# Optimization experiments

Measured on AMD Instinct MI355X. Metric: run time of the kernel, lower is better.

The kernel has to match this reference:

```python
import jax, jax.numpy as jnp
import numpy as np

B, T = 2, 2048
N_EMBED = 2048
N_HEAD = 16
N_KV_HEAD = 4
HEAD_DIM = N_EMBED // N_HEAD  # 128
KV_DIM = HEAD_DIM * N_KV_HEAD  # 512
REPEAT = N_HEAD // N_KV_HEAD  # 4
THETA = 10000.0


def _apply_rope(x):
    # x: (B, T, H, D), interleaved-pair rotation as in RotaryEmbedding
    D = x.shape[-1]
    inv_freq = 1.0 / (THETA ** (jnp.arange(0, D, 2, dtype=jnp.float32) / D))  # (D/2,)
    t = jnp.arange(x.shape[1], dtype=jnp.float32)
    freqs = t[:, None] * inv_freq[None, :]            # (T, D/2)
    cos = jnp.cos(freqs)[None, :, None, :]            # (1, T, 1, D/2)
    sin = jnp.sin(freqs)[None, :, None, :]
    x1 = x[..., ::2]
    x2 = x[..., 1::2]
    even = x1 * cos - x2 * sin
    odd = x1 * sin + x2 * cos
    out = jnp.stack([even, odd], axis=-1)             # (B, T, H, D/2, 2)
    return out.reshape(x.shape)


def setup_inputs() -> dict:
    key = jax.random.key(0)
    ks = jax.random.split(key, 9)
    s_in = 1.0 / np.sqrt(N_EMBED)
    return {
        "x": jax.random.normal(ks[0], (B, T, N_EMBED), dtype=jnp.float32),
        "Wq": jax.random.normal(ks[1], (N_EMBED, N_EMBED), dtype=jnp.float32) * s_in,
        "bq": jax.random.normal(ks[2], (N_EMBED,), dtype=jnp.float32) * 0.01,
        "Wk": jax.random.normal(ks[3], (KV_DIM, N_EMBED), dtype=jnp.float32) * s_in,
        "bk": jax.random.normal(ks[4], (KV_DIM,), dtype=jnp.float32) * 0.01,
        "Wv": jax.random.normal(ks[5], (KV_DIM, N_EMBED), dtype=jnp.float32) * s_in,
        "bv": jax.random.normal(ks[6], (KV_DIM,), dtype=jnp.float32) * 0.01,
        "Wo": jax.random.normal(ks[7], (N_EMBED, N_EMBED), dtype=jnp.float32) * s_in,
        "bo": jax.random.normal(ks[8], (N_EMBED,), dtype=jnp.float32) * 0.01,
    }


def reference(x, Wq, bq, Wk, bk, Wv, bv, Wo, bo):
    Bb, Tt, _ = x.shape
    q = (x @ Wq.T + bq).reshape(Bb, Tt, N_HEAD, HEAD_DIM)
    k = (x @ Wk.T + bk).reshape(Bb, Tt, N_KV_HEAD, HEAD_DIM)
    v = (x @ Wv.T + bv).reshape(Bb, Tt, N_KV_HEAD, HEAD_DIM)
    xq = _apply_rope(q).transpose(0, 2, 1, 3)          # (B, H, T, D)
    xk = _apply_rope(k).transpose(0, 2, 1, 3)          # (B, Hkv, T, D)
    xv = v.transpose(0, 2, 1, 3)
    if REPEAT > 1:
        xk = jnp.repeat(xk, REPEAT, axis=1)            # (B, H, T, D)
        xv = jnp.repeat(xv, REPEAT, axis=1)
    qk = jnp.einsum('bhqd,bhkd->bhqk', xq, xk)         # NOTE: no pre-softmax scale (faithful)
    causal = jnp.tril(jnp.ones((Tt, Tt), dtype=bool))
    qk = jnp.where(causal[None, None, :, :], qk, -jnp.inf)
    attn = jax.nn.softmax(qk, axis=-1) * (N_EMBED ** -0.5)  # post-softmax scale, faithful to source
    o = jnp.einsum('bhqk,bhkd->bhqd', attn, xv)
    o = o.transpose(0, 2, 1, 3).reshape(Bb, Tt, N_EMBED)
    return o @ Wo.T + bo
```

## Files before the change

kernel.cpp:

```cpp
#include <hip/hip_runtime.h>
#include <math.h>


typedef __bf16 bf16;
typedef __bf16 bf16x8 __attribute__((ext_vector_type(8)));
typedef __bf16 bf16x4 __attribute__((ext_vector_type(4)));
typedef __bf16 bf16x2 __attribute__((ext_vector_type(2)));
typedef float  f32x4  __attribute__((ext_vector_type(4)));

#define T_SEQ 2048
#define NE    2048
#define NH    16
#define NKVH  4
#define HD    128
#define KVD   512
#define OSCALE 0.022097086912079608f

__device__ __forceinline__ void gload16(const void* g, void* l) {
  __builtin_amdgcn_global_load_lds(
      (const __attribute__((address_space(1))) void*)g,
      (__attribute__((address_space(3))) void*)l, 16, 0, 0);
}

__global__ __launch_bounds__(256) void prep_convert(
    const float* __restrict__ x,  const float* __restrict__ wq,
    const float* __restrict__ wk, const float* __restrict__ wv,
    const float* __restrict__ wo,
    bf16* __restrict__ xb,  bf16* __restrict__ wqb, bf16* __restrict__ wkb,
    bf16* __restrict__ wvb, bf16* __restrict__ wob)
{
  const size_t total4 = (size_t)(8388608 + 4194304 + 1048576 + 1048576 + 4194304) / 4;
  for (size_t i = (size_t)blockIdx.x * blockDim.x + threadIdx.x; i < total4;
       i += (size_t)gridDim.x * blockDim.x) {
    size_t e = i * 4;
    const float* s; bf16* d; size_t off;
    if      (e <  8388608u) { s = x;  d = xb;  off = e; }
    else if (e < 12582912u) { s = wq; d = wqb; off = e -  8388608u; }
    else if (e < 13631488u) { s = wk; d = wkb; off = e - 12582912u; }
    else if (e < 14680064u) { s = wv; d = wvb; off = e - 13631488u; }
    else                    { s = wo; d = wob; off = e - 14680064u; }
    float4 v = *(const float4*)(s + off);
    bf16x4 o = {(bf16)v.x, (bf16)v.y, (bf16)v.z, (bf16)v.w};
    *(bf16x4*)(d + off) = o;
  }
}

__global__ __launch_bounds__(256) void rope_init(float2* __restrict__ rope)
{
  int i = blockIdx.x * 256 + threadIdx.x;
  int t = i >> 6, p = i & 63;
  float invf = powf(10000.f, -(float)p * (1.f / 64.f));
  double frd = (double)((float)t * invf);
  rope[i] = make_float2((float)cos(frd), (float)sin(frd));
}

__device__ __forceinline__ void mfma_gemm_128(
    const bf16* __restrict__ Ag,
    const bf16* __restrict__ Bg,
    f32x4 acc[4][4])
{
  __shared__ bf16 As[128][32];
  __shared__ bf16 Bs[128][32];
  const int tid  = threadIdx.x;
  const int wave = tid >> 6, lane = tid & 63;
  const int g = lane >> 4, c = lane & 15;
  const int wm = wave >> 1, wn = wave & 1;

  const f32x4 zf = {0.f, 0.f, 0.f, 0.f};
  #pragma unroll
  for (int mi = 0; mi < 4; ++mi)
    #pragma unroll
    for (int ni = 0; ni < 4; ++ni) acc[mi][ni] = zf;

  const int lr = lane >> 2;
  const int lc = (lane & 3) * 8;
  const bf16* aG0 = Ag + (size_t)(wave * 16 + lr) * NE + lc;
  const bf16* aG1 = aG0 + (size_t)64 * NE;
  const bf16* bG0 = Bg + (size_t)(wave * 16 + lr) * NE + lc;
  const bf16* bG1 = bG0 + (size_t)64 * NE;
  bf16* aL0 = &As[wave * 16][0];
  bf16* aL1 = &As[64 + wave * 16][0];
  bf16* bL0 = &Bs[wave * 16][0];
  bf16* bL1 = &Bs[64 + wave * 16][0];

  for (int k0 = 0; k0 < NE; k0 += 32) {
    __syncthreads();
    gload16(aG0 + k0, aL0);
    gload16(aG1 + k0, aL1);
    gload16(bG0 + k0, bL0);
    gload16(bG1 + k0, bL1);
    __syncthreads();
    bf16x8 af[4], bfr[4];
    #pragma unroll
    for (int mi = 0; mi < 4; ++mi)
      af[mi] = *(const bf16x8*)&As[wm * 64 + mi * 16 + c][g * 8];
    #pragma unroll
    for (int ni = 0; ni < 4; ++ni)
      bfr[ni] = *(const bf16x8*)&Bs[wn * 64 + ni * 16 + c][g * 8];
    #pragma unroll
    for (int mi = 0; mi < 4; ++mi)
      #pragma unroll
      for (int ni = 0; ni < 4; ++ni)
        acc[mi][ni] = __builtin_amdgcn_mfma_f32_16x16x32_bf16(
            af[mi], bfr[ni], acc[mi][ni], 0, 0, 0);
  }
}

__device__ __forceinline__ int xcd_swz(int bid, int nwg) {
  return (bid & 7) * (nwg >> 3) + (bid >> 3);
}

__global__ __launch_bounds__(256) void qkv_mfma(
    const bf16* __restrict__ xb,  const bf16* __restrict__ wqb,
    const bf16* __restrict__ wkb, const bf16* __restrict__ wvb,
    const float* __restrict__ bq, const float* __restrict__ bk,
    const float* __restrict__ bv, const float2* __restrict__ rope,
    bf16* __restrict__ q_ws, bf16* __restrict__ k_ws, bf16* __restrict__ vT_ws)
{
  const int wid = xcd_swz(blockIdx.x, 768);
  const int n0 = (wid % 24) * 128;
  const int m0 = (wid / 24) * 128;
  int region; const bf16* Wp; const float* bp; int nl0;
  if (n0 < NE)            { region = 0; Wp = wqb; bp = bq; nl0 = n0; }
  else if (n0 < NE + KVD) { region = 1; Wp = wkb; bp = bk; nl0 = n0 - NE; }
  else                    { region = 2; Wp = wvb; bp = bv; nl0 = n0 - NE - KVD; }

  f32x4 acc[4][4];
  mfma_gemm_128(xb + (size_t)m0 * NE, Wp + (size_t)nl0 * NE, acc);

  const int tid = threadIdx.x, wave = tid >> 6, lane = tid & 63;
  const int g = lane >> 4, c = lane & 15;
  const int wm = wave >> 1, wn = wave & 1;
  const int bbase = m0 >> 11;
  const int t0base = (m0 & (T_SEQ - 1)) + wm * 64;

  if (region < 2) {
    bf16* dst = (region == 0) ? q_ws : k_ws;
    const int nheads_stride = (region == 0) ? NH : NKVH;
    #pragma unroll
    for (int ni = 0; ni < 4; ++ni) {
      const int nloc = nl0 + wn * 64 + ni * 16 + c;
      const float bias = bp[nloc];
      const int d  = nloc & (HD - 1);
      const int p  = d >> 1;
      const int hh = nloc >> 7;
      const size_t base = ((size_t)bbase * nheads_stride + hh) * (size_t)T_SEQ * HD;
      #pragma unroll
      for (int mi = 0; mi < 4; ++mi) {
        #pragma unroll
        for (int r = 0; r < 4; ++r) {
          const int t = t0base + mi * 16 + g * 4 + r;
          float val = acc[mi][ni][r] + bias;
          float other = __shfl_xor(val, 1);
          float2 cs = rope[t * 64 + p];
          float res = (c & 1) ? fmaf(other, cs.y, val * cs.x)
                              : fmaf(val, cs.x, -(other * cs.y));
          float rpair = __shfl_xor(res, 1);
          if (!(c & 1)) {
            bf16x2 pk = {(bf16)res, (bf16)rpair};
            *(bf16x2*)&dst[base + (size_t)t * HD + d] = pk;
          }
        }
      }
    }
  } else {
    #pragma unroll
    for (int ni = 0; ni < 4; ++ni) {
      const int nloc = nl0 + wn * 64 + ni * 16 + c;
      const float bias = bp[nloc];
      const int d  = nloc & (HD - 1);
      const int hh = nloc >> 7;
      const size_t vrow = ((size_t)bbase * NKVH + hh) * HD + d;
      #pragma unroll
      for (int mi = 0; mi < 4; ++mi) {
        const int t0 = t0base + mi * 16 + g * 4;
        bf16x4 pk = {(bf16)(acc[mi][ni][0] + bias), (bf16)(acc[mi][ni][1] + bias),
                     (bf16)(acc[mi][ni][2] + bias), (bf16)(acc[mi][ni][3] + bias)};
        *(bf16x4*)&vT_ws[vrow * T_SEQ + t0] = pk;
      }
    }
  }
}

__global__ __launch_bounds__(256) void attn_mfma(
    const bf16* __restrict__ q_ws, const bf16* __restrict__ k_ws,
    const bf16* __restrict__ vT_ws, bf16* __restrict__ o_ws)
{
  __shared__ bf16 Ks[64][136];
  __shared__ bf16 Vs[128][72];
  __shared__ bf16 Ps[4][16][72];

  const int tid = threadIdx.x, wave = tid >> 6, lane = tid & 63;
  const int g = lane >> 4, c = lane & 15;
  const int qt = blockIdx.x, h = blockIdx.y, b = blockIdx.z;
  const int kvh = h >> 2;

  const bf16* Qg = q_ws + (((size_t)b * NH + h) * T_SEQ + qt * 64 + wave * 16) * HD;
  const bf16* Kg = k_ws + ((size_t)b * NKVH + kvh) * (size_t)T_SEQ * HD;
  const bf16* Vg = vT_ws + ((size_t)b * NKVH + kvh) * (size_t)HD * T_SEQ;

  bf16x8 qf[4];
  #pragma unroll
  for (int kc = 0; kc < 4; ++kc)
    qf[kc] = *(const bf16x8*)(Qg + (size_t)c * HD + kc * 32 + g * 8);

  const f32x4 zf = {0.f, 0.f, 0.f, 0.f};
  f32x4 o_acc[8];
  #pragma unroll
  for (int i = 0; i < 8; ++i) o_acc[i] = zf;

  float m_run[4], l_run[4];
  #pragma unroll
  for (int r = 0; r < 4; ++r) { m_run[r] = -1e30f; l_run[r] = 0.f; }

  const int qrow_base = qt * 64 + wave * 16 + g * 4;
  const int k_srow = tid >> 4, k_schunk = tid & 15;
  const int v_srow = tid >> 3, v_schunk = tid & 7;
  const int nkt = qt + 1;

  for (int kt = 0; kt < nkt; ++kt) {
    const int kb0 = kt * 64;
    __syncthreads();
    #pragma unroll
    for (int i = 0; i < 4; ++i) {
      int row = k_srow + i * 16;
      bf16x8 v = *(const bf16x8*)(Kg + (size_t)(kb0 + row) * HD + k_schunk * 8);
      *(bf16x8*)&Ks[row][k_schunk * 8] = v;
    }
    #pragma unroll
    for (int i = 0; i < 4; ++i) {
      int d = v_srow + i * 32;
      bf16x8 v = *(const bf16x8*)(Vg + (size_t)d * T_SEQ + kb0 + v_schunk * 8);
      *(bf16x8*)&Vs[d][v_schunk * 8] = v;
    }
    __syncthreads();

    f32x4 s[4];
    #pragma unroll
    for (int cf = 0; cf < 4; ++cf) s[cf] = zf;
    #pragma unroll
    for (int cf = 0; cf < 4; ++cf)
      #pragma unroll
      for (int kc = 0; kc < 4; ++kc) {
        bf16x8 kf = *(const bf16x8*)&Ks[cf * 16 + c][kc * 32 + g * 8];
        s[cf] = __builtin_amdgcn_mfma_f32_16x16x32_bf16(qf[kc], kf, s[cf], 0, 0, 0);
      }

    if (kt == qt) {
      #pragma unroll
      for (int cf = 0; cf < 4; ++cf) {
        int key = kb0 + cf * 16 + c;
        #pragma unroll
        for (int r = 0; r < 4; ++r)
          if (key > qrow_base + r) s[cf][r] = -1e30f;
      }
    }

    float corr[4], mx[4];
    #pragma unroll
    for (int r = 0; r < 4; ++r) {
      float m2 = fmaxf(fmaxf(s[0][r], s[1][r]), fmaxf(s[2][r], s[3][r]));
      m2 = fmaxf(m2, __shfl_xor(m2, 1));
      m2 = fmaxf(m2, __shfl_xor(m2, 2));
      m2 = fmaxf(m2, __shfl_xor(m2, 4));
      m2 = fmaxf(m2, __shfl_xor(m2, 8));
      float mn = fmaxf(m_run[r], m2);
      corr[r] = __expf(m_run[r] - mn);
      m_run[r] = mn;
      mx[r] = mn;
    }
    float rs[4] = {0.f, 0.f, 0.f, 0.f};
    #pragma unroll
    for (int cf = 0; cf < 4; ++cf)
      #pragma unroll
      for (int r = 0; r < 4; ++r) {
        float p = __expf(s[cf][r] - mx[r]);
        s[cf][r] = p;
        rs[r] += p;
      }
    #pragma unroll
    for (int r = 0; r < 4; ++r) {
      float t = rs[r];
      t += __shfl_xor(t, 1); t += __shfl_xor(t, 2);
      t += __shfl_xor(t, 4); t += __shfl_xor(t, 8);
      l_run[r] = l_run[r] * corr[r] + t;
    }

    #pragma unroll
    for (int cf = 0; cf < 4; ++cf)
      #pragma unroll
      for (int r = 0; r < 4; ++r)
        Ps[wave][g * 4 + r][cf * 16 + c] = (bf16)s[cf][r];

    #pragma unroll
    for (int d0 = 0; d0 < 8; ++d0)
      #pragma unroll
      for (int r = 0; r < 4; ++r)
        o_acc[d0][r] *= corr[r];

    bf16x8 pa0 = *(const bf16x8*)&Ps[wave][c][g * 8];
    bf16x8 pa1 = *(const bf16x8*)&Ps[wave][c][32 + g * 8];
    #pragma unroll
    for (int d0 = 0; d0 < 8; ++d0) {
      bf16x8 v0 = *(const bf16x8*)&Vs[d0 * 16 + c][g * 8];
      bf16x8 v1 = *(const bf16x8*)&Vs[d0 * 16 + c][32 + g * 8];
      o_acc[d0] = __builtin_amdgcn_mfma_f32_16x16x32_bf16(pa0, v0, o_acc[d0], 0, 0, 0);
      o_acc[d0] = __builtin_amdgcn_mfma_f32_16x16x32_bf16(pa1, v1, o_acc[d0], 0, 0, 0);
    }
  }

  float f[4];
  #pragma unroll
  for (int r = 0; r < 4; ++r) f[r] = OSCALE / l_run[r];
  #pragma unroll
  for (int d0 = 0; d0 < 8; ++d0)
    #pragma unroll
    for (int r = 0; r < 4; ++r) {
      float val = o_acc[d0][r] * f[r];
      float pv = __shfl_xor(val, 1);
      if (!(c & 1)) {
        bf16x2 pk = {(bf16)val, (bf16)pv};
        size_t row = (size_t)b * T_SEQ + qt * 64 + wave * 16 + g * 4 + r;
        int col = h * HD + d0 * 16 + c;
        *(bf16x2*)&o_ws[row * NE + col] = pk;
      }
    }
}

__global__ __launch_bounds__(256) void out_proj_mfma(
    const bf16* __restrict__ ob, const bf16* __restrict__ wob,
    const float* __restrict__ bo, float* __restrict__ out)
{
  const int wid = xcd_swz(blockIdx.x, 512);
  const int n0 = (wid % 16) * 128;
  const int m0 = (wid / 16) * 128;
  f32x4 acc[4][4];
  mfma_gemm_128(ob + (size_t)m0 * NE, wob + (size_t)n0 * NE, acc);

  const int tid = threadIdx.x, wave = tid >> 6, lane = tid & 63;
  const int g = lane >> 4, c = lane & 15;
  const int wm = wave >> 1, wn = wave & 1;
  #pragma unroll
  for (int ni = 0; ni < 4; ++ni) {
    const int n = n0 + wn * 64 + ni * 16 + c;
    const float bias = bo[n];
    #pragma unroll
    for (int mi = 0; mi < 4; ++mi)
      #pragma unroll
      for (int r = 0; r < 4; ++r) {
        const int m = m0 + wm * 64 + mi * 16 + g * 4 + r;
        out[(size_t)m * NE + n] = acc[mi][ni][r] + bias;
      }
  }
}

extern "C" void kernel_launch(void* const* d_in, const int* in_sizes, int n_in,
                              void* d_out, int out_size, void* d_ws, size_t ws_size,
                              hipStream_t stream)
{
  const float* x  = (const float*)d_in[0];
  const float* Wq = (const float*)d_in[1];
  const float* bq = (const float*)d_in[2];
  const float* Wk = (const float*)d_in[3];
  const float* bk = (const float*)d_in[4];
  const float* Wv = (const float*)d_in[5];
  const float* bv = (const float*)d_in[6];
  const float* Wo = (const float*)d_in[7];
  const float* bo = (const float*)d_in[8];
  float* out = (float*)d_out;

  bf16* xb    = (bf16*)d_ws;
  bf16* wqb   = xb    + 8388608;
  bf16* wkb   = wqb   + 4194304;
  bf16* wvb   = wkb   + 1048576;
  bf16* wob   = wvb   + 1048576;
  bf16* q_ws  = wob   + 4194304;
  bf16* k_ws  = q_ws  + 8388608;
  bf16* vT_ws = k_ws  + 2097152;
  bf16* o_ws  = vT_ws + 2097152;
  float2* rope = (float2*)(o_ws + 8388608);

  prep_convert<<<2048, 256, 0, stream>>>(x, Wq, Wk, Wv, Wo, xb, wqb, wkb, wvb, wob);
  rope_init<<<512, 256, 0, stream>>>(rope);
  qkv_mfma<<<768, 256, 0, stream>>>(xb, wqb, wkb, wvb, bq, bk, bv, rope,
                                    q_ws, k_ws, vT_ws);
  attn_mfma<<<dim3(32, 16, 2), 256, 0, stream>>>(q_ws, k_ws, vT_ws, o_ws);
  out_proj_mfma<<<512, 256, 0, stream>>>(o_ws, wob, bo, out);
}
```

Baseline: 456.5 us.

## Swizzle attention LDS tiles, remap causal block order, raise occupancy and MFMA priority

Replaces the padded shared-memory K, V and P tiles with unpadded byte buffers addressed through an XOR swizzle, which cuts bank conflicts and shrinks the LDS footprint. The attention launch becomes a flat 1D grid remapped so query tiles are issued as 0..15 and then 31 down to 16, aiming for better causal load balance. It also adds launch_bounds with a minimum of 4 blocks and s_setprio around the MFMA loops. The risks are register pressure from the occupancy hint and the swizzle math adding address ALU work.

```diff
diff --git a/kernel.cpp b/kernel.cpp
--- a/kernel.cpp
+++ b/kernel.cpp
@@ -182,17 +182,21 @@
   }
 }
 
-__global__ __launch_bounds__(256) void attn_mfma(
+__global__ __launch_bounds__(256, 4) void attn_mfma(
     const bf16* __restrict__ q_ws, const bf16* __restrict__ k_ws,
     const bf16* __restrict__ vT_ws, bf16* __restrict__ o_ws)
 {
-  __shared__ bf16 Ks[64][136];
-  __shared__ bf16 Vs[128][72];
-  __shared__ bf16 Ps[4][16][72];
+  __shared__ __align__(16) char smem[40960];
+  char* Ks = smem;
+  char* Vs = smem + 16384;
+  char* Ps = smem + 32768;
 
   const int tid = threadIdx.x, wave = tid >> 6, lane = tid & 63;
   const int g = lane >> 4, c = lane & 15;
-  const int qt = blockIdx.x, h = blockIdx.y, b = blockIdx.z;
+  const int bid = blockIdx.x;
+  const int u = bid & 31, v = bid >> 5;
+  const int h = u & 15, b = u >> 4;
+  const int qt = (v < 16) ? v : (47 - v);
   const int kvh = h >> 2;
 
   const bf16* Qg = q_ws + (((size_t)b * NH + h) * T_SEQ + qt * 64 + wave * 16) * HD;
@@ -214,8 +218,11 @@
   for (int r = 0; r < 4; ++r) { m_run[r] = -1e30f; l_run[r] = 0.f; }
 
   const int qrow_base = qt * 64 + wave * 16 + g * 4;
-  const int k_srow = tid >> 4, k_schunk = tid & 15;
-  const int v_srow = tid >> 3, v_schunk = tid & 7;
+  const int ks_row = tid >> 4;
+  const int ks_cb  = (tid & 15) * 16;
+  const int vs_row = tid >> 3;
+  const int vs_cb  = (tid & 7) * 16;
+  const int swzc   = (c & 7) << 4;
   const int nkt = qt + 1;
 
   for (int kt = 0; kt < nkt; ++kt) {
@@ -223,28 +230,31 @@
     __syncthreads();
     #pragma unroll
     for (int i = 0; i < 4; ++i) {
-      int row = k_srow + i * 16;
-      bf16x8 v = *(const bf16x8*)(Kg + (size_t)(kb0 + row) * HD + k_schunk * 8);
-      *(bf16x8*)&Ks[row][k_schunk * 8] = v;
+      int row = ks_row + i * 16;
+      bf16x8 vv = *(const bf16x8*)(Kg + (size_t)(kb0 + row) * HD + (ks_cb >> 1));
+      *(bf16x8*)(Ks + row * 256 + (ks_cb ^ ((row & 7) << 4))) = vv;
     }
     #pragma unroll
     for (int i = 0; i < 4; ++i) {
-      int d = v_srow + i * 32;
-      bf16x8 v = *(const bf16x8*)(Vg + (size_t)d * T_SEQ + kb0 + v_schunk * 8);
-      *(bf16x8*)&Vs[d][v_schunk * 8] = v;
+      int d = vs_row + i * 32;
+      bf16x8 vv = *(const bf16x8*)(Vg + (size_t)d * T_SEQ + kb0 + (vs_cb >> 1));
+      *(bf16x8*)(Vs + d * 128 + (vs_cb ^ ((d & 7) << 4))) = vv;
     }
     __syncthreads();
 
     f32x4 s[4];
     #pragma unroll
     for (int cf = 0; cf < 4; ++cf) s[cf] = zf;
+    __builtin_amdgcn_s_setprio(1);
     #pragma unroll
     for (int cf = 0; cf < 4; ++cf)
       #pragma unroll
       for (int kc = 0; kc < 4; ++kc) {
-        bf16x8 kf = *(const bf16x8*)&Ks[cf * 16 + c][kc * 32 + g * 8];
+        bf16x8 kf = *(const bf16x8*)(Ks + (cf * 16 + c) * 256 +
+                                     ((kc * 64 + g * 16) ^ swzc));
         s[cf] = __builtin_amdgcn_mfma_f32_16x16x32_bf16(qf[kc], kf, s[cf], 0, 0, 0);
       }
+    __builtin_amdgcn_s_setprio(0);
 
     if (kt == qt) {
       #pragma unroll
@@ -286,11 +296,15 @@
       l_run[r] = l_run[r] * corr[r] + t;
     }
 
+    char* Pw = Ps + wave * 2048;
     #pragma unroll
     for (int cf = 0; cf < 4; ++cf)
       #pragma unroll
-      for (int r = 0; r < 4; ++r)
-        Ps[wave][g * 4 + r][cf * 16 + c] = (bf16)s[cf][r];
+      for (int r = 0; r < 4; ++r) {
+        int row = g * 4 + r;
+        *(bf16*)(Pw + row * 128 + (((cf * 16 + c) * 2) ^ ((row & 7) << 4))) =
+            (bf16)s[cf][r];
+      }
 
     #pragma unroll
     for (int d0 = 0; d0 < 8; ++d0)
@@ -298,15 +312,17 @@
       for (int r = 0; r < 4; ++r)
         o_acc[d0][r] *= corr[r];
 
-    bf16x8 pa0 = *(const bf16x8*)&Ps[wave][c][g * 8];
-    bf16x8 pa1 = *(const bf16x8*)&Ps[wave][c][32 + g * 8];
+    bf16x8 pa0 = *(const bf16x8*)(Pw + c * 128 + ((g * 16) ^ swzc));
+    bf16x8 pa1 = *(const bf16x8*)(Pw + c * 128 + ((64 + g * 16) ^ swzc));
+    __builtin_amdgcn_s_setprio(1);
     #pragma unroll
     for (int d0 = 0; d0 < 8; ++d0) {
-      bf16x8 v0 = *(const bf16x8*)&Vs[d0 * 16 + c][g * 8];
-      bf16x8 v1 = *(const bf16x8*)&Vs[d0 * 16 + c][32 + g * 8];
+      bf16x8 v0 = *(const bf16x8*)(Vs + (d0 * 16 + c) * 128 + ((g * 16) ^ swzc));
+      bf16x8 v1 = *(const bf16x8*)(Vs + (d0 * 16 + c) * 128 + ((64 + g * 16) ^ swzc));
       o_acc[d0] = __builtin_amdgcn_mfma_f32_16x16x32_bf16(pa0, v0, o_acc[d0], 0, 0, 0);
       o_acc[d0] = __builtin_amdgcn_mfma_f32_16x16x32_bf16(pa1, v1, o_acc[d0], 0, 0, 0);
     }
+    __builtin_amdgcn_s_setprio(0);
   }
 
   float f[4];
@@ -384,6 +400,6 @@
   rope_init<<<512, 256, 0, stream>>>(rope);
   qkv_mfma<<<768, 256, 0, stream>>>(xb, wqb, wkb, wvb, bq, bk, bv, rope,
                                     q_ws, k_ws, vT_ws);
-  attn_mfma<<<dim3(32, 16, 2), 256, 0, stream>>>(q_ws, k_ws, vT_ws, o_ws);
+  attn_mfma<<<1024, 256, 0, stream>>>(q_ws, k_ws, vT_ws, o_ws);
   out_proj_mfma<<<512, 256, 0, stream>>>(o_ws, wob, bo, out);
 }
```

After: 449.9 us. Within noise of the previous version (-1.4%).
